# Kernel tuning notes

Measured on AMD Instinct MI355X. Metric: run time of the kernel, lower is better.

## Reference

```python
import jax, jax.numpy as jnp
import numpy as np

N = 100000   # nodes
E = 1600000  # edges (avg degree 16)
D = 128      # in_dim == hidden
L = 3        # num_layers
G = 512      # graphs in batch


def setup_inputs() -> dict:
    key = jax.random.key(0)
    ks = jax.random.split(key, 14)
    s = 0.05
    return {
        "x": jax.random.normal(ks[0], (N, D), jnp.float32),
        "edge_index": jax.random.randint(ks[1], (2, E), 0, N, dtype=jnp.int32),
        "batch": jnp.sort(jax.random.randint(ks[2], (N,), 0, G, dtype=jnp.int32)),
        "W1": jax.random.normal(ks[3], (L, D, D), jnp.float32) * s,
        "b1": jax.random.normal(ks[4], (L, D), jnp.float32) * s,
        "W2": jax.random.normal(ks[5], (L, D, D), jnp.float32) * s,
        "b2": jax.random.normal(ks[6], (L, D), jnp.float32) * s,
        "gamma": jax.random.uniform(ks[7], (L, D), jnp.float32, 0.5, 1.5),
        "beta": jax.random.normal(ks[8], (L, D), jnp.float32) * s,
        "run_mean": jax.random.normal(ks[9], (L, D), jnp.float32) * s,
        "run_var": jax.random.uniform(ks[10], (L, D), jnp.float32, 0.5, 1.5),
        "eps": jnp.zeros((L,), jnp.float32),
        "lin1_W": jax.random.normal(ks[11], (D, D), jnp.float32) * s,
        "lin1_b": jax.random.normal(ks[12], (D,), jnp.float32) * s,
    }


def _bn(h, g, b, m, v):
    # BatchNorm1d in eval mode (running stats)
    return (h - m) * jax.lax.rsqrt(v + 1e-5) * g + b


def reference(x, edge_index, batch, W1, b1, W2, b2, gamma, beta,
              run_mean, run_var, eps, lin1_W, lin1_b):
    n = x.shape[0]
    src, dst = edge_index[0], edge_index[1]
    h = x
    for l in range(L):  # small fixed layer count
        # GINConv: sum-aggregate neighbor features then (1+eps)*self + agg
        agg = jax.ops.segment_sum(h[src], dst, num_segments=n)  # [N, D]
        z = (1.0 + eps[l]) * h + agg
        z = jax.nn.relu(z @ W1[l] + b1[l])
        z = jax.nn.relu(z @ W2[l] + b2[l])
        h = _bn(z, gamma[l], beta[l], run_mean[l], run_var[l])
    # global_mean_pool over graph ids
    counts = jax.ops.segment_sum(jnp.ones((n,), h.dtype), batch, num_segments=G)
    pooled = jax.ops.segment_sum(h, batch, num_segments=G)
    pooled = pooled / jnp.maximum(counts, 1.0)[:, None]  # [G, D]
    # lin1 + ReLU (dropout is identity in eval)
    return jax.nn.relu(pooled @ lin1_W + lin1_b)
```

## Files before the change

kernel.cpp:

```cpp
#include <hip/hip_runtime.h>
#include <hip/hip_bf16.h>

#define NN 100000
#define NE 1600000
#define DD 128
#define NL 3
#define NG 512
#define CSRP (NE + 8 * NN)
#define BSHIFT 9
#define NBUCK2 ((NN + 511) / 512)
#define ABLKS 512
#define ECHUNK (NE / ABLKS)

#define CONV_BLKS 12501
#define PREPW_BLKS 384
#define INIT_BLKS (CONV_BLKS + PREPW_BLKS + 1)

typedef __attribute__((ext_vector_type(8))) short bf16x8;
typedef __attribute__((ext_vector_type(4))) float f32x4;

__device__ __forceinline__ unsigned short f2bf(float f) {
    union { float f; unsigned int u; } x; x.f = f;
    unsigned int r = x.u + 0x7FFFu + ((x.u >> 16) & 1u);
    return (unsigned short)(r >> 16);
}
__device__ __forceinline__ float bf2f(unsigned short u) {
    union { unsigned int u; float f; } x; x.u = ((unsigned int)u) << 16;
    return x.f;
}
__device__ __forceinline__ float bflo(unsigned int v) { return bf2f((unsigned short)(v & 0xffffu)); }
__device__ __forceinline__ float bfhi(unsigned int v) { return bf2f((unsigned short)(v >> 16)); }
__device__ __forceinline__ unsigned cvtpk(float lo, float hi) {
    unsigned r;
    asm("v_cvt_pk_bf16_f32 %0, %1, %2" : "=v"(r) : "v"(lo), "v"(hi));
    return r;
}

__global__ __launch_bounds__(256) void init_all(const float* __restrict__ x,
                                                unsigned short* __restrict__ h0,
                                                unsigned short* __restrict__ h1,
                                                const float* __restrict__ W1,
                                                const float* __restrict__ W2,
                                                unsigned short* __restrict__ wbf,
                                                int* __restrict__ bcnt) {
    int bb = blockIdx.x;
    if (bb < CONV_BLKS) {
        long long t = (long long)bb * 256 + threadIdx.x;
        long long base = t * 4;
        if (base < (long long)NN * DD) {
            float4 v = *reinterpret_cast<const float4*>(x + base);
            ushort4 p;
            p.x = f2bf(v.x); p.y = f2bf(v.y); p.z = f2bf(v.z); p.w = f2bf(v.w);
            *reinterpret_cast<ushort4*>(h0 + base) = p;
        } else if (base < (long long)(NN + 1) * DD) {
            ushort4 z = {0, 0, 0, 0};
            *reinterpret_cast<ushort4*>(h0 + base) = z;
            *reinterpret_cast<ushort4*>(h1 + base) = z;
        }
        return;
    }
    bb -= CONV_BLKS;
    if (bb < PREPW_BLKS) {
        int idx = bb * 256 + threadIdx.x;
        int k = idx & 127;
        int n = (idx >> 7) & 127;
        int w = (idx >> 14) & 1;
        int l = idx >> 15;
        const float* src = w ? W2 : W1;
        wbf[idx] = f2bf(src[(l * DD + k) * DD + n]);
        return;
    }
    int i = threadIdx.x;
    if (i < NBUCK2) bcnt[i] = 0;
}

__global__ __launch_bounds__(256) void bcount(const int* __restrict__ ei,
                                              int* __restrict__ bcnt) {
    __shared__ int hist[NBUCK2];
    int tid = threadIdx.x;
    int e0 = blockIdx.x * ECHUNK;
    for (int i = tid; i < NBUCK2; i += 256) hist[i] = 0;
    __syncthreads();
    for (int i = tid; i < ECHUNK; i += 256)
        atomicAdd(&hist[ei[NE + e0 + i] >> BSHIFT], 1);
    __syncthreads();
    for (int i = tid; i < NBUCK2; i += 256) {
        int h = hist[i];
        if (h) atomicAdd(&bcnt[i], h);
    }
}

__global__ __launch_bounds__(256) void bscan(const int* __restrict__ bcnt,
                                             int* __restrict__ cboff,
                                             int* __restrict__ gpos) {
    __shared__ int s[256];
    int tid = threadIdx.x;
    int sum = (tid < NBUCK2) ? bcnt[tid] : 0;
    s[tid] = sum;
    __syncthreads();
    for (int o = 1; o < 256; o <<= 1) {
        int t = (tid >= o) ? s[tid - o] : 0;
        __syncthreads();
        s[tid] += t;
        __syncthreads();
    }
    if (tid < NBUCK2) {
        cboff[tid] = s[tid] - sum;
        gpos[tid] = 0;
    }
    if (tid == 0) cboff[NBUCK2] = NE;
}

__global__ __launch_bounds__(256) void binA(const int* __restrict__ ei,
                                            const int* __restrict__ cboff,
                                            int* __restrict__ gpos,
                                            int* __restrict__ ebuf) {
    __shared__ int hist[NBUCK2];
    __shared__ int sbase[NBUCK2];
    int tid = threadIdx.x;
    int e0 = blockIdx.x * ECHUNK;
    for (int i = tid; i < NBUCK2; i += 256) hist[i] = 0;
    __syncthreads();
    for (int i = tid; i < ECHUNK; i += 256) {
        int d = ei[NE + e0 + i];
        atomicAdd(&hist[d >> BSHIFT], 1);
    }
    __syncthreads();
    for (int i = tid; i < NBUCK2; i += 256) {
        int h = hist[i];
        sbase[i] = (h > 0) ? atomicAdd(&gpos[i], h) : 0;
        hist[i] = 0;
    }
    __syncthreads();
    for (int i = tid; i < ECHUNK; i += 256) {
        int s2 = ei[e0 + i];
        int d = ei[NE + e0 + i];
        int b = d >> BSHIFT;
        int pos = atomicAdd(&hist[b], 1);
        ebuf[cboff[b] + sbase[b] + pos] = s2 | ((d & 511) << 17);
    }
}

__global__ __launch_bounds__(256) void bpre(const int* __restrict__ ebuf,
                                            const int* __restrict__ cboff,
                                            int* __restrict__ rp,
                                            int* __restrict__ bsum) {
    __shared__ int lcnt[512];
    __shared__ int s[256];
    int b = blockIdx.x;
    int tid = threadIdx.x;
    lcnt[tid] = 0;
    lcnt[tid + 256] = 0;
    __syncthreads();
    int st = cboff[b], en = cboff[b + 1];
    for (int i = st + tid; i < en; i += 256)
        atomicAdd(&lcnt[ebuf[i] >> 17], 1);
    __syncthreads();
    int d0 = (lcnt[2 * tid] + 7) & ~7;
    int d1 = (lcnt[2 * tid + 1] + 7) & ~7;
    int ps = d0 + d1;
    s[tid] = ps;
    __syncthreads();
    for (int o = 1; o < 256; o <<= 1) {
        int t = (tid >= o) ? s[tid - o] : 0;
        __syncthreads();
        s[tid] += t;
        __syncthreads();
    }
    int base = s[tid] - ps;
    int node0 = (b << BSHIFT) + 2 * tid;
    if (node0 < NN) rp[node0] = base;
    if (node0 + 1 < NN) rp[node0 + 1] = base + d0;
    if (tid == 255) bsum[b] = s[255];
}

__global__ __launch_bounds__(256) void bscan2(const int* __restrict__ bsum,
                                              int* __restrict__ bbase,
                                              int* __restrict__ rp) {
    __shared__ int s[256];
    int tid = threadIdx.x;
    int sum = (tid < NBUCK2) ? bsum[tid] : 0;
    s[tid] = sum;
    __syncthreads();
    for (int o = 1; o < 256; o <<= 1) {
        int t = (tid >= o) ? s[tid - o] : 0;
        __syncthreads();
        s[tid] += t;
        __syncthreads();
    }
    if (tid < NBUCK2) bbase[tid] = s[tid] - sum;
    if (tid == 255) rp[NN] = s[255];
}

__global__ __launch_bounds__(256) void binB2(const int* __restrict__ ebuf,
                                             const int* __restrict__ cboff,
                                             const int* __restrict__ bbase,
                                             int* __restrict__ rp,
                                             int* __restrict__ csr) {
    __shared__ int rpl[512];
    __shared__ int lcnt[512];
    int b = blockIdx.x;
    int tid = threadIdx.x;
    int bb = bbase[b];
    for (int i = tid; i < 512; i += 256) {
        int node = (b << BSHIFT) + i;
        int v = 0;
        if (node < NN) {
            v = rp[node] + bb;
            rp[node] = v;
        }
        rpl[i] = v;
        lcnt[i] = 0;
    }
    __syncthreads();
    int st = cboff[b], en = cboff[b + 1];
    for (int i = st + tid; i < en; i += 256) {
        int v = ebuf[i];
        int dl = v >> 17;
        int pos = atomicAdd(&lcnt[dl], 1);
        csr[rpl[dl] + pos] = v & 0x1FFFF;
    }
    __syncthreads();
    for (int i = tid; i < 512; i += 256) {
        int node = (b << BSHIFT) + i;
        if (node >= NN) continue;
        int d = lcnt[i];
        int pd = (d + 7) & ~7;
        int base = rpl[i];
        for (int j = d; j < pd; ++j) csr[base + j] = NN;
    }
}

__global__ __launch_bounds__(256) void layer_fused(
    const unsigned short* __restrict__ hin,
    const int* __restrict__ rp,
    const int* __restrict__ csr,
    const unsigned short* __restrict__ w1t,
    const unsigned short* __restrict__ w2t,
    const float* __restrict__ b1,
    const float* __restrict__ b2,
    const float* __restrict__ gamma,
    const float* __restrict__ beta,
    const float* __restrict__ rmean,
    const float* __restrict__ rvar,
    const float* __restrict__ epsv,
    unsigned short* __restrict__ hout)
{
    __shared__ unsigned short z_lds[16 * 136];
    const int tid = threadIdx.x;
    const int lane = tid & 63;
    const int wave = tid >> 6;
    const int gid = lane >> 4;
    const int lg = lane & 15;
    const int row0 = blockIdx.x * 16;
    const float epl = 1.0f + epsv[0];
    const size_t lgo = (size_t)lg * 8;

#define ACC8(v) do { \
    acc[0] += bflo((v).x); acc[1] += bfhi((v).x); \
    acc[2] += bflo((v).y); acc[3] += bfhi((v).y); \
    acc[4] += bflo((v).z); acc[5] += bfhi((v).z); \
    acc[6] += bflo((v).w); acc[7] += bfhi((v).w); } while (0)

    const int rbase = row0 + (wave << 2);
    int pv = (lane < 5) ? rp[rbase + lane] : 0;
    const int st = __shfl(pv, gid);
    const int en = __shfl(pv, gid + 1);
    const int myrow = rbase + gid;

    float acc[8];
    {
        uint4 sv = *reinterpret_cast<const uint4*>(hin + (size_t)myrow * DD + lgo);
        acc[0] = epl * bflo(sv.x); acc[1] = epl * bfhi(sv.x);
        acc[2] = epl * bflo(sv.y); acc[3] = epl * bfhi(sv.y);
        acc[4] = epl * bflo(sv.z); acc[5] = epl * bfhi(sv.z);
        acc[6] = epl * bflo(sv.w); acc[7] = epl * bfhi(sv.w);
    }
    int c0 = st;
    for (; c0 + 16 <= en; c0 += 16) {
        int4 idA = *reinterpret_cast<const int4*>(csr + c0);
        int4 idB = *reinterpret_cast<const int4*>(csr + c0 + 4);
        int4 idC = *reinterpret_cast<const int4*>(csr + c0 + 8);
        int4 idD = *reinterpret_cast<const int4*>(csr + c0 + 12);
        uint4 v0 = *reinterpret_cast<const uint4*>(hin + (size_t)idA.x * DD + lgo);
        uint4 v1 = *reinterpret_cast<const uint4*>(hin + (size_t)idA.y * DD + lgo);
        uint4 v2 = *reinterpret_cast<const uint4*>(hin + (size_t)idA.z * DD + lgo);
        uint4 v3 = *reinterpret_cast<const uint4*>(hin + (size_t)idA.w * DD + lgo);
        uint4 v4 = *reinterpret_cast<const uint4*>(hin + (size_t)idB.x * DD + lgo);
        uint4 v5 = *reinterpret_cast<const uint4*>(hin + (size_t)idB.y * DD + lgo);
        uint4 v6 = *reinterpret_cast<const uint4*>(hin + (size_t)idB.z * DD + lgo);
        uint4 v7 = *reinterpret_cast<const uint4*>(hin + (size_t)idB.w * DD + lgo);
        uint4 v8 = *reinterpret_cast<const uint4*>(hin + (size_t)idC.x * DD + lgo);
        uint4 v9 = *reinterpret_cast<const uint4*>(hin + (size_t)idC.y * DD + lgo);
        uint4 va = *reinterpret_cast<const uint4*>(hin + (size_t)idC.z * DD + lgo);
        uint4 vb = *reinterpret_cast<const uint4*>(hin + (size_t)idC.w * DD + lgo);
        uint4 vc = *reinterpret_cast<const uint4*>(hin + (size_t)idD.x * DD + lgo);
        uint4 vd = *reinterpret_cast<const uint4*>(hin + (size_t)idD.y * DD + lgo);
        uint4 ve = *reinterpret_cast<const uint4*>(hin + (size_t)idD.z * DD + lgo);
        uint4 vf = *reinterpret_cast<const uint4*>(hin + (size_t)idD.w * DD + lgo);
        ACC8(v0); ACC8(v1); ACC8(v2); ACC8(v3);
        ACC8(v4); ACC8(v5); ACC8(v6); ACC8(v7);
        ACC8(v8); ACC8(v9); ACC8(va); ACC8(vb);
        ACC8(vc); ACC8(vd); ACC8(ve); ACC8(vf);
    }
    if (c0 < en) {
        int4 idA = *reinterpret_cast<const int4*>(csr + c0);
        int4 idB = *reinterpret_cast<const int4*>(csr + c0 + 4);
        uint4 v0 = *reinterpret_cast<const uint4*>(hin + (size_t)idA.x * DD + lgo);
        uint4 v1 = *reinterpret_cast<const uint4*>(hin + (size_t)idA.y * DD + lgo);
        uint4 v2 = *reinterpret_cast<const uint4*>(hin + (size_t)idA.z * DD + lgo);
        uint4 v3 = *reinterpret_cast<const uint4*>(hin + (size_t)idA.w * DD + lgo);
        uint4 v4 = *reinterpret_cast<const uint4*>(hin + (size_t)idB.x * DD + lgo);
        uint4 v5 = *reinterpret_cast<const uint4*>(hin + (size_t)idB.y * DD + lgo);
        uint4 v6 = *reinterpret_cast<const uint4*>(hin + (size_t)idB.z * DD + lgo);
        uint4 v7 = *reinterpret_cast<const uint4*>(hin + (size_t)idB.w * DD + lgo);
        ACC8(v0); ACC8(v1); ACC8(v2); ACC8(v3);
        ACC8(v4); ACC8(v5); ACC8(v6); ACC8(v7);
    }
    {
        uint4 pk;
        pk.x = cvtpk(acc[0], acc[1]);
        pk.y = cvtpk(acc[2], acc[3]);
        pk.z = cvtpk(acc[4], acc[5]);
        pk.w = cvtpk(acc[6], acc[7]);
        *reinterpret_cast<uint4*>(&z_lds[((wave << 2) + gid) * 136 + lg * 8]) = pk;
    }
    __syncthreads();

    const int l15 = lane & 15;
    const int kq = lane >> 4;
    const int colbase = wave << 5;

    bf16x8 afr[4];
    #pragma unroll
    for (int kk = 0; kk < 4; ++kk)
        afr[kk] = *reinterpret_cast<const bf16x8*>(&z_lds[l15 * 136 + kk * 32 + kq * 8]);
    __syncthreads();

    f32x4 acc4[2];
    #pragma unroll
    for (int nt = 0; nt < 2; ++nt) acc4[nt] = (f32x4){0.f, 0.f, 0.f, 0.f};
    #pragma unroll
    for (int nt = 0; nt < 2; ++nt) {
        #pragma unroll
        for (int kk = 0; kk < 4; ++kk) {
            bf16x8 bfr = *reinterpret_cast<const bf16x8*>(
                w1t + (colbase + nt * 16 + l15) * DD + kk * 32 + kq * 8);
            acc4[nt] = __builtin_amdgcn_mfma_f32_16x16x32_bf16(afr[kk], bfr, acc4[nt], 0, 0, 0);
        }
    }

    #pragma unroll
    for (int nt = 0; nt < 2; ++nt) {
        int col = colbase + nt * 16 + l15;
        float bv = b1[col];
        #pragma unroll
        for (int r = 0; r < 4; ++r) {
            int zr = kq * 4 + r;
            float v = acc4[nt][r] + bv;
            v = v > 0.f ? v : 0.f;
            z_lds[zr * 136 + col] = f2bf(v);
        }
    }
    __syncthreads();

    #pragma unroll
    for (int kk = 0; kk < 4; ++kk)
        afr[kk] = *reinterpret_cast<const bf16x8*>(&z_lds[l15 * 136 + kk * 32 + kq * 8]);
    #pragma unroll
    for (int nt = 0; nt < 2; ++nt) acc4[nt] = (f32x4){0.f, 0.f, 0.f, 0.f};
    #pragma unroll
    for (int nt = 0; nt < 2; ++nt) {
        #pragma unroll
        for (int kk = 0; kk < 4; ++kk) {
            bf16x8 bfr = *reinterpret_cast<const bf16x8*>(
                w2t + (colbase + nt * 16 + l15) * DD + kk * 32 + kq * 8);
            acc4[nt] = __builtin_amdgcn_mfma_f32_16x16x32_bf16(afr[kk], bfr, acc4[nt], 0, 0, 0);
        }
    }

    #pragma unroll
    for (int nt = 0; nt < 2; ++nt) {
        int col = colbase + nt * 16 + l15;
        float bv = b2[col];
        float ga = gamma[col];
        float be = beta[col];
        float mu = rmean[col];
        float inv = rsqrtf(rvar[col] + 1e-5f);
        #pragma unroll
        for (int r = 0; r < 4; ++r) {
            int zr = kq * 4 + r;
            float v = acc4[nt][r] + bv;
            v = v > 0.f ? v : 0.f;
            v = (v - mu) * inv * ga + be;
            hout[(size_t)(row0 + zr) * DD + col] = f2bf(v);
        }
    }
#undef ACC8
}

__global__ __launch_bounds__(256) void pool_final(const unsigned short* __restrict__ h,
                                                  const int* __restrict__ batch,
                                                  const float* __restrict__ W,
                                                  const float* __restrict__ b,
                                                  float* __restrict__ out) {
    int g = blockIdx.x;
    int t = threadIdx.x;
    int c2 = t & 63;
    int qu = t >> 6;

    int lo = 0, hi = NN;
    while (lo < hi) { int mid = (lo + hi) >> 1; if (batch[mid] < g) lo = mid + 1; else hi = mid; }
    int start = lo;
    hi = NN;
    while (lo < hi) { int mid = (lo + hi) >> 1; if (batch[mid] < g + 1) lo = mid + 1; else hi = mid; }
    int end = lo;

    float ax = 0.f, ay = 0.f;
    for (int i = start + qu; i < end; i += 4) {
        unsigned u = *reinterpret_cast<const unsigned*>(h + (size_t)i * DD + c2 * 2);
        ax += bflo(u); ay += bfhi(u);
    }

    __shared__ float ps[4][DD];
    ps[qu][c2 * 2] = ax;
    ps[qu][c2 * 2 + 1] = ay;
    __syncthreads();
    if (t < DD) {
        float inv = 1.0f / fmaxf((float)(end - start), 1.0f);
        ps[0][t] = (ps[0][t] + ps[1][t] + ps[2][t] + ps[3][t]) * inv;
    }
    __syncthreads();
    if (t < DD) {
        float o = b[t];
        #pragma unroll 8
        for (int k = 0; k < DD; ++k)
            o += ps[0][k] * W[k * DD + t];
        out[(size_t)g * DD + t] = fmaxf(o, 0.f);
    }
}

extern "C" void kernel_launch(void* const* d_in, const int* in_sizes, int n_in,
                              void* d_out, int out_size, void* d_ws, size_t ws_size,
                              hipStream_t stream) {
    const float* x     = (const float*)d_in[0];
    const int*   ei    = (const int*)d_in[1];
    const int*   batch = (const int*)d_in[2];
    const float* W1    = (const float*)d_in[3];
    const float* b1    = (const float*)d_in[4];
    const float* W2    = (const float*)d_in[5];
    const float* b2    = (const float*)d_in[6];
    const float* gamma = (const float*)d_in[7];
    const float* beta  = (const float*)d_in[8];
    const float* rmean = (const float*)d_in[9];
    const float* rvar  = (const float*)d_in[10];
    const float* eps   = (const float*)d_in[11];
    const float* lin1W = (const float*)d_in[12];
    const float* lin1b = (const float*)d_in[13];
    float* out = (float*)d_out;

    char* ws = (char*)d_ws;
    size_t off = 0;
    auto alloc = [&](size_t bytes) {
        void* p = ws + off;
        off = (off + bytes + 255) & ~(size_t)255;
        return p;
    };
    unsigned short* h0  = (unsigned short*)alloc((size_t)(NN + 1) * DD * 2);
    unsigned short* h1  = (unsigned short*)alloc((size_t)(NN + 1) * DD * 2);
    int* rp    = (int*)alloc((size_t)(NN + 1) * 4);
    int* bcnt  = (int*)alloc((size_t)NBUCK2 * 4);
    int* cboff = (int*)alloc((size_t)(NBUCK2 + 1) * 4);
    int* gpos  = (int*)alloc((size_t)NBUCK2 * 4);
    int* bsum  = (int*)alloc((size_t)NBUCK2 * 4);
    int* bbase = (int*)alloc((size_t)NBUCK2 * 4);
    int* csr   = (int*)alloc((size_t)CSRP * 4);
    int* ebuf  = (int*)alloc((size_t)NE * 4);
    unsigned short* wbf = (unsigned short*)alloc((size_t)NL * 2 * DD * DD * 2);

    init_all<<<INIT_BLKS, 256, 0, stream>>>(x, h0, h1, W1, W2, wbf, bcnt);

    bcount<<<ABLKS, 256, 0, stream>>>(ei, bcnt);
    bscan<<<1, 256, 0, stream>>>(bcnt, cboff, gpos);
    binA<<<ABLKS, 256, 0, stream>>>(ei, cboff, gpos, ebuf);
    bpre<<<NBUCK2, 256, 0, stream>>>(ebuf, cboff, rp, bsum);
    bscan2<<<1, 256, 0, stream>>>(bsum, bbase, rp);
    binB2<<<NBUCK2, 256, 0, stream>>>(ebuf, cboff, bbase, rp, csr);

    const int lgrid = NN / 16;
    layer_fused<<<lgrid, 256, 0, stream>>>(
        h0, rp, csr, wbf + 0 * DD * DD, wbf + 1 * DD * DD,
        b1 + 0 * DD, b2 + 0 * DD, gamma + 0 * DD, beta + 0 * DD,
        rmean + 0 * DD, rvar + 0 * DD, eps + 0, h1);
    layer_fused<<<lgrid, 256, 0, stream>>>(
        h1, rp, csr, wbf + 2 * DD * DD, wbf + 3 * DD * DD,
        b1 + 1 * DD, b2 + 1 * DD, gamma + 1 * DD, beta + 1 * DD,
        rmean + 1 * DD, rvar + 1 * DD, eps + 1, h0);
    layer_fused<<<lgrid, 256, 0, stream>>>(
        h0, rp, csr, wbf + 4 * DD * DD, wbf + 5 * DD * DD,
        b1 + 2 * DD, b2 + 2 * DD, gamma + 2 * DD, beta + 2 * DD,
        rmean + 2 * DD, rvar + 2 * DD, eps + 2, h1);

    pool_final<<<NG, 256, 0, stream>>>(h1, batch, lin1W, lin1b, out);
}
```

Baseline: 473.5 us.

## Replace atomic bucket offsets with per-block histogram scan and simplify gather loop

```diff
diff --git a/kernel.cpp b/kernel.cpp
--- a/kernel.cpp
+++ b/kernel.cpp
@@ -14,7 +14,7 @@
 
 #define CONV_BLKS 12501
 #define PREPW_BLKS 384
-#define INIT_BLKS (CONV_BLKS + PREPW_BLKS + 1)
+#define INIT_BLKS (CONV_BLKS + PREPW_BLKS + ABLKS)
 
 typedef __attribute__((ext_vector_type(8))) short bf16x8;
 typedef __attribute__((ext_vector_type(4))) float f32x4;
@@ -42,10 +42,12 @@
                                                 const float* __restrict__ W1,
                                                 const float* __restrict__ W2,
                                                 unsigned short* __restrict__ wbf,
-                                                int* __restrict__ bcnt) {
+                                                const int* __restrict__ ei,
+                                                int* __restrict__ blkhist) {
     int bb = blockIdx.x;
+    int tid = threadIdx.x;
     if (bb < CONV_BLKS) {
-        long long t = (long long)bb * 256 + threadIdx.x;
+        long long t = (long long)bb * 256 + tid;
         long long base = t * 4;
         if (base < (long long)NN * DD) {
             float4 v = *reinterpret_cast<const float4*>(x + base);
@@ -61,7 +63,7 @@
     }
     bb -= CONV_BLKS;
     if (bb < PREPW_BLKS) {
-        int idx = bb * 256 + threadIdx.x;
+        int idx = bb * 256 + tid;
         int k = idx & 127;
         int n = (idx >> 7) & 127;
         int w = (idx >> 14) & 1;
@@ -70,74 +72,80 @@
         wbf[idx] = f2bf(src[(l * DD + k) * DD + n]);
         return;
     }
-    int i = threadIdx.x;
-    if (i < NBUCK2) bcnt[i] = 0;
-}
-
-__global__ __launch_bounds__(256) void bcount(const int* __restrict__ ei,
-                                              int* __restrict__ bcnt) {
-    __shared__ int hist[NBUCK2];
-    int tid = threadIdx.x;
-    int e0 = blockIdx.x * ECHUNK;
-    for (int i = tid; i < NBUCK2; i += 256) hist[i] = 0;
-    __syncthreads();
-    for (int i = tid; i < ECHUNK; i += 256)
-        atomicAdd(&hist[ei[NE + e0 + i] >> BSHIFT], 1);
-    __syncthreads();
-    for (int i = tid; i < NBUCK2; i += 256) {
-        int h = hist[i];
-        if (h) atomicAdd(&bcnt[i], h);
-    }
-}
-
-__global__ __launch_bounds__(256) void bscan(const int* __restrict__ bcnt,
-                                             int* __restrict__ cboff,
-                                             int* __restrict__ gpos) {
+    bb -= PREPW_BLKS;
+    {
+        __shared__ int hist[NBUCK2];
+        for (int i = tid; i < NBUCK2; i += 256) hist[i] = 0;
+        __syncthreads();
+        int e0 = bb * ECHUNK;
+        for (int i = tid; i < ECHUNK; i += 256)
+            atomicAdd(&hist[ei[NE + e0 + i] >> BSHIFT], 1);
+        __syncthreads();
+        for (int i = tid; i < NBUCK2; i += 256)
+            blkhist[i * ABLKS + bb] = hist[i];
+    }
+}
+
+__global__ __launch_bounds__(256) void scanA(int* __restrict__ blkhist,
+                                             int* __restrict__ bsumb) {
     __shared__ int s[256];
-    int tid = threadIdx.x;
-    int sum = (tid < NBUCK2) ? bcnt[tid] : 0;
+    int b = blockIdx.x;
+    int tid = threadIdx.x;
+    int* row = blkhist + (size_t)b * ABLKS;
+    int v0 = row[2 * tid];
+    int v1 = row[2 * tid + 1];
+    int ps = v0 + v1;
+    s[tid] = ps;
+    __syncthreads();
+    for (int o = 1; o < 256; o <<= 1) {
+        int t2 = (tid >= o) ? s[tid - o] : 0;
+        __syncthreads();
+        s[tid] += t2;
+        __syncthreads();
+    }
+    int base = s[tid] - ps;
+    row[2 * tid] = base;
+    row[2 * tid + 1] = base + v0;
+    if (tid == 255) bsumb[b] = s[255];
+}
+
+__global__ __launch_bounds__(256) void scanB(const int* __restrict__ bsumb,
+                                             int* __restrict__ cboff) {
+    __shared__ int s[256];
+    int tid = threadIdx.x;
+    int sum = (tid < NBUCK2) ? bsumb[tid] : 0;
     s[tid] = sum;
     __syncthreads();
     for (int o = 1; o < 256; o <<= 1) {
-        int t = (tid >= o) ? s[tid - o] : 0;
-        __syncthreads();
-        s[tid] += t;
-        __syncthreads();
-    }
+        int t2 = (tid >= o) ? s[tid - o] : 0;
+        __syncthreads();
+        s[tid] += t2;
+        __syncthreads();
+    }
+    if (tid < NBUCK2) cboff[tid] = s[tid] - sum;
+    if (tid == 0) cboff[NBUCK2] = NE;
+}
+
+__global__ __launch_bounds__(256) void binA2(const int* __restrict__ ei,
+                                             const int* __restrict__ cboff,
+                                             const int* __restrict__ blkhist,
+                                             int* __restrict__ ebuf) {
+    __shared__ int lbase[NBUCK2];
+    __shared__ int cur[NBUCK2];
+    int tid = threadIdx.x;
+    int bid = blockIdx.x;
     if (tid < NBUCK2) {
-        cboff[tid] = s[tid] - sum;
-        gpos[tid] = 0;
-    }
-    if (tid == 0) cboff[NBUCK2] = NE;
-}
-
-__global__ __launch_bounds__(256) void binA(const int* __restrict__ ei,
-                                            const int* __restrict__ cboff,
-                                            int* __restrict__ gpos,
-                                            int* __restrict__ ebuf) {
-    __shared__ int hist[NBUCK2];
-    __shared__ int sbase[NBUCK2];
-    int tid = threadIdx.x;
-    int e0 = blockIdx.x * ECHUNK;
-    for (int i = tid; i < NBUCK2; i += 256) hist[i] = 0;
-    __syncthreads();
-    for (int i = tid; i < ECHUNK; i += 256) {
-        int d = ei[NE + e0 + i];
-        atomicAdd(&hist[d >> BSHIFT], 1);
-    }
-    __syncthreads();
-    for (int i = tid; i < NBUCK2; i += 256) {
-        int h = hist[i];
-        sbase[i] = (h > 0) ? atomicAdd(&gpos[i], h) : 0;
-        hist[i] = 0;
-    }
-    __syncthreads();
+        lbase[tid] = cboff[tid] + blkhist[tid * ABLKS + bid];
+        cur[tid] = 0;
+    }
+    __syncthreads();
+    int e0 = bid * ECHUNK;
     for (int i = tid; i < ECHUNK; i += 256) {
         int s2 = ei[e0 + i];
         int d = ei[NE + e0 + i];
         int b = d >> BSHIFT;
-        int pos = atomicAdd(&hist[b], 1);
-        ebuf[cboff[b] + sbase[b] + pos] = s2 | ((d & 511) << 17);
+        int pos = atomicAdd(&cur[b], 1);
+        ebuf[lbase[b] + pos] = s2 | ((d & 511) << 17);
     }
 }
 
@@ -162,9 +170,9 @@
     s[tid] = ps;
     __syncthreads();
     for (int o = 1; o < 256; o <<= 1) {
-        int t = (tid >= o) ? s[tid - o] : 0;
-        __syncthreads();
-        s[tid] += t;
+        int t2 = (tid >= o) ? s[tid - o] : 0;
+        __syncthreads();
+        s[tid] += t2;
         __syncthreads();
     }
     int base = s[tid] - ps;
@@ -183,9 +191,9 @@
     s[tid] = sum;
     __syncthreads();
     for (int o = 1; o < 256; o <<= 1) {
-        int t = (tid >= o) ? s[tid - o] : 0;
-        __syncthreads();
-        s[tid] += t;
+        int t2 = (tid >= o) ? s[tid - o] : 0;
+        __syncthreads();
+        s[tid] += t2;
         __syncthreads();
     }
     if (tid < NBUCK2) bbase[tid] = s[tid] - sum;
@@ -276,34 +284,7 @@
         acc[4] = epl * bflo(sv.z); acc[5] = epl * bfhi(sv.z);
         acc[6] = epl * bflo(sv.w); acc[7] = epl * bfhi(sv.w);
     }
-    int c0 = st;
-    for (; c0 + 16 <= en; c0 += 16) {
-        int4 idA = *reinterpret_cast<const int4*>(csr + c0);
-        int4 idB = *reinterpret_cast<const int4*>(csr + c0 + 4);
-        int4 idC = *reinterpret_cast<const int4*>(csr + c0 + 8);
-        int4 idD = *reinterpret_cast<const int4*>(csr + c0 + 12);
-        uint4 v0 = *reinterpret_cast<const uint4*>(hin + (size_t)idA.x * DD + lgo);
-        uint4 v1 = *reinterpret_cast<const uint4*>(hin + (size_t)idA.y * DD + lgo);
-        uint4 v2 = *reinterpret_cast<const uint4*>(hin + (size_t)idA.z * DD + lgo);
-        uint4 v3 = *reinterpret_cast<const uint4*>(hin + (size_t)idA.w * DD + lgo);
-        uint4 v4 = *reinterpret_cast<const uint4*>(hin + (size_t)idB.x * DD + lgo);
-        uint4 v5 = *reinterpret_cast<const uint4*>(hin + (size_t)idB.y * DD + lgo);
-        uint4 v6 = *reinterpret_cast<const uint4*>(hin + (size_t)idB.z * DD + lgo);
-        uint4 v7 = *reinterpret_cast<const uint4*>(hin + (size_t)idB.w * DD + lgo);
-        uint4 v8 = *reinterpret_cast<const uint4*>(hin + (size_t)idC.x * DD + lgo);
-        uint4 v9 = *reinterpret_cast<const uint4*>(hin + (size_t)idC.y * DD + lgo);
-        uint4 va = *reinterpret_cast<const uint4*>(hin + (size_t)idC.z * DD + lgo);
-        uint4 vb = *reinterpret_cast<const uint4*>(hin + (size_t)idC.w * DD + lgo);
-        uint4 vc = *reinterpret_cast<const uint4*>(hin + (size_t)idD.x * DD + lgo);
-        uint4 vd = *reinterpret_cast<const uint4*>(hin + (size_t)idD.y * DD + lgo);
-        uint4 ve = *reinterpret_cast<const uint4*>(hin + (size_t)idD.z * DD + lgo);
-        uint4 vf = *reinterpret_cast<const uint4*>(hin + (size_t)idD.w * DD + lgo);
-        ACC8(v0); ACC8(v1); ACC8(v2); ACC8(v3);
-        ACC8(v4); ACC8(v5); ACC8(v6); ACC8(v7);
-        ACC8(v8); ACC8(v9); ACC8(va); ACC8(vb);
-        ACC8(vc); ACC8(vd); ACC8(ve); ACC8(vf);
-    }
-    if (c0 < en) {
+    for (int c0 = st; c0 < en; c0 += 8) {
         int4 idA = *reinterpret_cast<const int4*>(csr + c0);
         int4 idB = *reinterpret_cast<const int4*>(csr + c0 + 4);
         uint4 v0 = *reinterpret_cast<const uint4*>(hin + (size_t)idA.x * DD + lgo);
@@ -468,21 +449,20 @@
     };
     unsigned short* h0  = (unsigned short*)alloc((size_t)(NN + 1) * DD * 2);
     unsigned short* h1  = (unsigned short*)alloc((size_t)(NN + 1) * DD * 2);
-    int* rp    = (int*)alloc((size_t)(NN + 1) * 4);
-    int* bcnt  = (int*)alloc((size_t)NBUCK2 * 4);
-    int* cboff = (int*)alloc((size_t)(NBUCK2 + 1) * 4);
-    int* gpos  = (int*)alloc((size_t)NBUCK2 * 4);
-    int* bsum  = (int*)alloc((size_t)NBUCK2 * 4);
-    int* bbase = (int*)alloc((size_t)NBUCK2 * 4);
-    int* csr   = (int*)alloc((size_t)CSRP * 4);
-    int* ebuf  = (int*)alloc((size_t)NE * 4);
+    int* rp      = (int*)alloc((size_t)(NN + 1) * 4);
+    int* blkhist = (int*)alloc((size_t)NBUCK2 * ABLKS * 4);
+    int* bsumb   = (int*)alloc((size_t)NBUCK2 * 4);
+    int* cboff   = (int*)alloc((size_t)(NBUCK2 + 1) * 4);
+    int* bsum    = (int*)alloc((size_t)NBUCK2 * 4);
+    int* bbase   = (int*)alloc((size_t)NBUCK2 * 4);
+    int* csr     = (int*)alloc((size_t)CSRP * 4);
+    int* ebuf    = (int*)alloc((size_t)NE * 4);
     unsigned short* wbf = (unsigned short*)alloc((size_t)NL * 2 * DD * DD * 2);
 
-    init_all<<<INIT_BLKS, 256, 0, stream>>>(x, h0, h1, W1, W2, wbf, bcnt);
-
-    bcount<<<ABLKS, 256, 0, stream>>>(ei, bcnt);
-    bscan<<<1, 256, 0, stream>>>(bcnt, cboff, gpos);
-    binA<<<ABLKS, 256, 0, stream>>>(ei, cboff, gpos, ebuf);
+    init_all<<<INIT_BLKS, 256, 0, stream>>>(x, h0, h1, W1, W2, wbf, ei, blkhist);
+    scanA<<<NBUCK2, 256, 0, stream>>>(blkhist, bsumb);
+    scanB<<<1, 256, 0, stream>>>(bsumb, cboff);
+    binA2<<<ABLKS, 256, 0, stream>>>(ei, cboff, blkhist, ebuf);
     bpre<<<NBUCK2, 256, 0, stream>>>(ebuf, cboff, rp, bsum);
     bscan2<<<1, 256, 0, stream>>>(bsum, bbase, rp);
     binB2<<<NBUCK2, 256, 0, stream>>>(ebuf, cboff, bbase, rp, csr);
```

Result: faster. 456.4 us (-3.6%).
